# Optimization experiments

Measured on AMD Instinct MI355X. Metric: run time of the kernel, lower is better.

Reference implementation:

```python
import jax, jax.numpy as jnp
import numpy as np

N_FFT = 16
HOP = 4
PAD = N_FFT // 2  # center=True padding/trim, torch default


def _frame_idx(n_frames):
    # [n_frames, N_FFT] sample indices for framing / overlap-add
    return jnp.arange(n_frames)[:, None] * HOP + jnp.arange(N_FFT)[None, :]


def _istft(spec, window):
    # spec: complex [B, 9, T] onesided; matches torch.istft(center=True, onesided=True)
    B, _, T = spec.shape
    frames = jnp.fft.irfft(spec, n=N_FFT, axis=1)            # [B, 16, T]
    frames = jnp.transpose(frames, (0, 2, 1)) * window       # [B, T, 16] windowed
    idx = _frame_idx(T).reshape(-1)
    L = (T - 1) * HOP + N_FFT
    ola = jnp.zeros((B, L), frames.dtype).at[:, idx].add(frames.reshape(B, -1))
    wsq = jnp.broadcast_to(window**2, (T, N_FFT)).reshape(-1)
    env = jnp.zeros((L,), window.dtype).at[idx].add(wsq)      # window-square envelope
    Lout = (T - 1) * HOP                                      # torch output length, center=True
    return ola[:, PAD:PAD + Lout] / env[PAD:PAD + Lout]


def _stft(x, window):
    # matches torch.stft(center=True, pad_mode='reflect', onesided=True)
    B, L = x.shape
    xp = jnp.pad(x, ((0, 0), (PAD, PAD)), mode='reflect')
    T = 1 + L // HOP
    frames = xp[:, _frame_idx(T)] * window                    # [B, T, 16]
    return jnp.transpose(jnp.fft.rfft(frames, axis=-1), (0, 2, 1))  # [B, 9, T]


def _hann(n):
    k = jnp.arange(n, dtype=jnp.float32)
    return 0.5 * (1.0 - jnp.cos(2.0 * jnp.pi * k / n))  # periodic hann, torch default


def setup_inputs() -> dict:
    key = jax.random.key(0)
    magnitude = jax.random.uniform(key, (32, 9, 65536), dtype=jnp.float32)
    window = _hann(N_FFT)
    return {"magnitude": magnitude, "window": window}


def reference(magnitude, window):
    # 1) zero-phase istft
    spec0 = magnitude.astype(jnp.complex64)  # mag * exp(i*0)
    wav_i = _istft(spec0, window)
    # 2) stft -> extract phase
    S = _stft(wav_i, window)
    phase = jnp.arctan2(S.imag, S.real)      # torch.angle
    T = min(magnitude.shape[-1], phase.shape[-1])
    mag = magnitude[..., :T]
    ph = phase[..., :T]
    # 3) recombine and final istft
    spec = jax.lax.complex(mag * jnp.cos(ph), mag * jnp.sin(ph))
    return _istft(spec, window)
```

## Files before the change

kernel.cpp:

```cpp
#include <hip/hip_runtime.h>


#define KB    9
#define TFR   65536
#define LW    262140

#define C1f 0.9238795325112867f
#define C2f 0.7071067811865476f
#define C3f 0.3826834323650898f

#define W1 0.03806023374435663f
#define W2 0.14644660940672627f
#define W3 0.30865828381745514f
#define W4 0.5f
#define W5 0.6913417161825449f
#define W6 0.8535533905932737f
#define W7 0.9619397662556434f

#define TMIN   256
#define TMAX   65280
#define FPW    116
#define NWAVES 561
#define BXI    141
#define GX     (BXI + 2)
#define NBLK   (GX * 32)

#define TILE  1024
#define NW    1048
#define NCA   265
#define NFB   259
#define MSTR  265
#define FSTR  17
#define FSTEP (FSTR - 4)

typedef float v2f __attribute__((ext_vector_type(2)));
typedef float v4f __attribute__((ext_vector_type(4)));

static __device__ __forceinline__ v2f mk(float a, float b){ v2f r; r.x=a; r.y=b; return r; }
static __device__ __forceinline__ v2f sp(float c){ v2f r; r.x=c; r.y=c; return r; }
static __device__ __forceinline__ v2f vfma(v2f a, v2f b, v2f c){ return __builtin_elementwise_fma(a,b,c); }
static __device__ __forceinline__ v2f vfma(float a, v2f b, v2f c){ return __builtin_elementwise_fma(sp(a),b,c); }

static __device__ __forceinline__ float SHP(float x){
  int xi = __builtin_bit_cast(int, x);
  int r = __builtin_amdgcn_update_dpp(xi, xi, 0x130, 0xF, 0xF, false);
  return __builtin_bit_cast(float, r);
}
static __device__ __forceinline__ float SHM(float x){
  int xi = __builtin_bit_cast(int, x);
  int r = __builtin_amdgcn_update_dpp(xi, xi, 0x138, 0xF, 0xF, false);
  return __builtin_bit_cast(float, r);
}

static __device__ __forceinline__ void phase1(float m, float Sr, float Si,
                                              float& pr, float& pi){
  float r2 = fmaf(Sr,Sr, Si*Si);
  if (r2 > 0.f) {
    float rin = __builtin_amdgcn_rsqf(r2);
    float mr = m * rin;
    pr = mr * Sr; pi = mr * Si;
  } else { pr = m; pi = 0.f; }
}
static __device__ __forceinline__ void phasev(v2f m, v2f Sr, v2f Si, v2f& pr, v2f& pi){
  float prx, pix, pry, piy;
  phase1(m.x, Sr.x, Si.x, prx, pix);
  phase1(m.y, Sr.y, Si.y, pry, piy);
  pr = mk(prx, pry); pi = mk(pix, piy);
}

__device__ __constant__ float W2C[16] = {
  0.f, W1*W1, W2*W2, W3*W3, 0.25f, W5*W5, W6*W6, W7*W7,
  1.f, W7*W7, W6*W6, W5*W5, 0.25f, W3*W3, W2*W2, W1*W1 };

__global__ __launch_bounds__(256, 5) void istft_all(
    const float* __restrict__ mag, float* __restrict__ out)
{
  __shared__ float s_mag[KB * MSTR];
  __shared__ float s_fab[NCA * FSTR];
  __shared__ float s_wav[NW];

  const int tid = threadIdx.x;

  const unsigned lin = (unsigned)blockIdx.y * GX + blockIdx.x;
  const unsigned swz = (lin & 7u) * (NBLK / 8u) + (lin >> 3);
  const unsigned b   = swz / (unsigned)GX;
  const int      pos = (int)(swz - b * GX);

  const float* magb = mag + (size_t)b * (size_t)(KB * TFR);
  float* outb = out + (size_t)b * LW;

  if (pos >= 2) {
    const int lane = tid & 63;
    const int wv   = (pos - 2) * 4 + (tid >> 6);
    if (wv >= NWAVES) return;
    const int T0 = TMIN + wv * FPW;
    const int ta = T0 - 6 + 2 * lane;

    v2f R0 = *(const v2f*)(magb + 0*TFR + ta);
    v2f R1 = *(const v2f*)(magb + 1*TFR + ta);
    v2f R2 = *(const v2f*)(magb + 2*TFR + ta);
    v2f R3 = *(const v2f*)(magb + 3*TFR + ta);
    v2f R4 = *(const v2f*)(magb + 4*TFR + ta);
    v2f R5 = *(const v2f*)(magb + 5*TFR + ta);
    v2f R6 = *(const v2f*)(magb + 6*TFR + ta);
    v2f R7 = *(const v2f*)(magb + 7*TFR + ta);
    v2f R8 = *(const v2f*)(magb + 8*TFR + ta);

    v2f f1,f2,f3,f4,f5,f6,f7,f8;
    {
      v2f p1=R1+R7, m1=R1-R7, p2=R2+R6, m2=R2-R6, p3=R3+R5, m3=R3-R5;
      v2f tp=R0+R8, tm=R0-R8, d13=p1-p3;
      v2f E1 = vfma(2.f, vfma(C1f,m1, vfma(C2f,m2, sp(C3f)*m3)), tm);
      v2f E2 = vfma(2.f, vfma(C2f,d13, -R4), tp);
      v2f E3 = vfma(2.f, vfma(C3f,m1, vfma(-C2f,m2, sp(-C1f)*m3)), tm);
      v2f E4 = vfma(2.f, R4-p2, tp);
      v2f E5 = vfma(2.f, vfma(-C3f,m1, vfma(-C2f,m2, sp(C1f)*m3)), tm);
      v2f E6 = vfma(-2.f, vfma(C2f,d13, R4), tp);
      v2f E7 = vfma(2.f, vfma(-C1f,m1, vfma(C2f,m2, sp(-C3f)*m3)), tm);
      v2f E8 = vfma(2.f, ((p2+R4)-(p1+p3)), tp);
      f1=sp(W1)*E1; f2=sp(W2)*E2; f3=sp(W3)*E3; f4=sp(W4)*E4;
      f5=sp(W5)*E5; f6=sp(W6)*E6; f7=sp(W7)*E7; f8=E8;
    }

    v2f wc0, wc1, wc2, wc3;
    {
      float s4 = SHP(f4.x), s5 = SHP(f5.x), s6 = SHP(f6.x), s7 = SHP(f7.x);
      float a1x = SHP(f1.x), a1y = SHP(f1.y);
      float a2x = SHP(f2.x), a2y = SHP(f2.y);
      float a3x = SHP(f3.x), a3y = SHP(f3.y);
      float m1y = SHM(f1.y), m2y = SHM(f2.y), m3y = SHM(f3.y), m4y = SHM(f4.y);
      v2f f4p1 = mk(f4.y, s4), f5p1 = mk(f5.y, s5), f6p1 = mk(f6.y, s6), f7p1 = mk(f7.y, s7);
      v2f f1p2 = mk(a1x, a1y), f2p2 = mk(a2x, a2y), f3p2 = mk(a3x, a3y);
      v2f f1m1 = mk(m1y, f1.x), f2m1 = mk(m2y, f2.x), f3m1 = mk(m3y, f3.x), f4m1 = mk(m4y, f4.x);
      const v2f inv24 = sp(1.f/24.f);
      wc0 = (f4p1 + f8 + f4m1) * inv24;
      wc1 = (f1p2 + f5p1 + f7 + f3m1) * inv24;
      wc2 = (f2p2 + f6p1 + f6 + f2m1) * inv24;
      wc3 = (f3p2 + f7p1 + f5 + f1m1) * inv24;
    }

    v2f x1,x2,x3,x4,x5,x6,x7,x8w,x9,x10,x11,x12,x13,x14,x15;
    {
      float aw0y = SHM(wc0.y);
      float aw1x = SHM(wc1.x), aw1y = SHM(wc1.y);
      float aw2x = SHM(wc2.x), aw2y = SHM(wc2.y);
      float aw3x = SHM(wc3.x), aw3y = SHM(wc3.y);
      float pw0x = SHP(wc0.x), pw1x = SHP(wc1.x), pw2x = SHP(wc2.x), pw3x = SHP(wc3.x);
      x1  = mk(aw1x, aw1y); x2  = mk(aw2x, aw2y); x3  = mk(aw3x, aw3y);
      x4  = mk(aw0y, wc0.x); x5 = mk(aw1y, wc1.x); x6 = mk(aw2y, wc2.x); x7 = mk(aw3y, wc3.x);
      x8w = wc0; x9 = wc1; x10 = wc2; x11 = wc3;
      x12 = mk(wc0.y, pw0x); x13 = mk(wc1.y, pw1x); x14 = mk(wc2.y, pw2x); x15 = mk(wc3.y, pw3x);
    }
    x1=sp(W1)*x1; x2=sp(W2)*x2; x3=sp(W3)*x3; x4=sp(W4)*x4; x5=sp(W5)*x5;
    x6=sp(W6)*x6; x7=sp(W7)*x7; x9=sp(W7)*x9; x10=sp(W6)*x10; x11=sp(W5)*x11;
    x12=sp(W4)*x12; x13=sp(W3)*x13; x14=sp(W2)*x14; x15=sp(W1)*x15;

    v2f fc1,fc2,fc3,fc4,fc5,fc6,fc7,fc8,fc9,fc10,fc11,fc12,fc13,fc14,fc15;
    {
      v2f u1=x1+x15, vv1=x1-x15, u2=x2+x14, vv2=x2-x14, u3=x3+x13, vv3=x3-x13,
          u4=x4+x12, vv4=x4-x12, u5=x5+x11, vv5=x5-x11, u6=x6+x10, vv6=x6-x10,
          u7=x7+x9,  vv7=x7-x9;
      v2f P1=u1+u7, M1=u1-u7, P2=u2+u6, M2=u2-u6, P3=u3+u5, M3=u3-u5;
      v2f D13 = P1-P3;
      v2f Sr0 = x8w + ((P1+P2)+(P3+u4));
      v2f Sr1 = vfma(C1f,M1, vfma(C2f,M2, sp(C3f)*M3)) - x8w;
      v2f Sr2 = vfma(C2f,D13, x8w - u4);
      v2f Sr3 = vfma(C3f,M1, vfma(-C2f,M2, sp(-C1f)*M3)) - x8w;
      v2f Sr4 = (u4 - P2) + x8w;
      v2f Sr5 = vfma(-C3f,M1, vfma(-C2f,M2, sp(C1f)*M3)) - x8w;
      v2f Sr6 = vfma(-C2f,D13, x8w - u4);
      v2f Sr7 = vfma(-C1f,M1, vfma(C2f,M2, sp(-C3f)*M3)) - x8w;
      v2f Sr8 = x8w + ((P2+u4)-(P1+P3));
      v2f Q1=vv1+vv7, N1=vv1-vv7, Q2=vv2+vv6, N2=vv2-vv6, Q3=vv3+vv5, N3=vv3-vv5;
      v2f NN = N1+N3;
      v2f Si1 = -(vfma(C3f,Q1, vfma(C2f,Q2, sp(C1f)*Q3)) + vv4);
      v2f Si2 = -vfma(C2f,NN, N2);
      v2f Si3 = -(vfma(C1f,Q1, vfma(C2f,Q2, sp(-C3f)*Q3)) - vv4);
      v2f Si4 = N3 - N1;
      v2f Si5 = -(vfma(C1f,Q1, vfma(-C2f,Q2, sp(-C3f)*Q3)) + vv4);
      v2f Si6 = vfma(-C2f,NN, N2);
      v2f Si7 = -(vfma(C3f,Q1, vfma(-C2f,Q2, sp(C1f)*Q3)) - vv4);

      v2f pr0,pr1,pr2,pr3,pr4,pr5,pr6,pr7,pr8;
      v2f pi1,pi2,pi3,pi4,pi5,pi6,pi7;
      pr0 = mk((Sr0.x >= 0.f) ? R0.x : -R0.x,
               (Sr0.y >= 0.f) ? R0.y : -R0.y);
      phasev(R1, Sr1, Si1, pr1, pi1);
      phasev(R2, Sr2, Si2, pr2, pi2);
      phasev(R3, Sr3, Si3, pr3, pi3);
      phasev(R4, Sr4, Si4, pr4, pi4);
      phasev(R5, Sr5, Si5, pr5, pi5);
      phasev(R6, Sr6, Si6, pr6, pi6);
      phasev(R7, Sr7, Si7, pr7, pi7);
      pr8 = mk((Sr8.x >= 0.f) ? R8.x : -R8.x,
               (Sr8.y >= 0.f) ? R8.y : -R8.y);

      v2f ap1=pr1+pr7, bm1=pr1-pr7, ap2=pr2+pr6, bm2=pr2-pr6, ap3=pr3+pr5, bm3=pr3-pr5;
      v2f tp=pr0+pr8, tm=pr0-pr8, ed=ap1-ap3;
      v2f E1 = vfma(2.f, vfma(C1f,bm1, vfma(C2f,bm2, sp(C3f)*bm3)), tm);
      v2f E2 = vfma(2.f, vfma(C2f,ed, -pr4), tp);
      v2f E3 = vfma(2.f, vfma(C3f,bm1, vfma(-C2f,bm2, sp(-C1f)*bm3)), tm);
      v2f E4 = vfma(2.f, pr4-ap2, tp);
      v2f E5 = vfma(2.f, vfma(-C3f,bm1, vfma(-C2f,bm2, sp(C1f)*bm3)), tm);
      v2f E6 = vfma(-2.f, vfma(C2f,ed, pr4), tp);
      v2f E7 = vfma(2.f, vfma(-C1f,bm1, vfma(C2f,bm2, sp(-C3f)*bm3)), tm);
      v2f E8 = vfma(2.f, ((ap2+pr4)-(ap1+ap3)), tp);
      v2f q1=pi1+pi7, n1=pi1-pi7, q2=pi2+pi6, n2=pi2-pi6, q3=pi3+pi5, n3=pi3-pi5;
      v2f nn = n1+n3;
      v2f O1 = sp(-2.f)*(vfma(C3f,q1, vfma(C2f,q2, sp(C1f)*q3)) + pi4);
      v2f O2 = sp(-2.f)*vfma(C2f,nn, n2);
      v2f O3 = sp(-2.f)*(vfma(C1f,q1, vfma(C2f,q2, sp(-C3f)*q3)) - pi4);
      v2f O4 = sp(-2.f)*(n1-n3);
      v2f O5 = sp(-2.f)*(vfma(C1f,q1, vfma(-C2f,q2, sp(-C3f)*q3)) + pi4);
      v2f O6 = sp(-2.f)*vfma(C2f,nn, -n2);
      v2f O7 = sp(-2.f)*(vfma(C3f,q1, vfma(-C2f,q2, sp(C1f)*q3)) - pi4);

      fc1 = sp(W1)*(E1+O1); fc2 = sp(W2)*(E2+O2); fc3 = sp(W3)*(E3+O3); fc4 = sp(W4)*(E4+O4);
      fc5 = sp(W5)*(E5+O5); fc6 = sp(W6)*(E6+O6); fc7 = sp(W7)*(E7+O7); fc8 = E8;
      fc9  = sp(W7)*(E7-O7); fc10 = sp(W6)*(E6-O6); fc11 = sp(W5)*(E5-O5); fc12 = sp(W4)*(E4-O4);
      fc13 = sp(W3)*(E3-O3); fc14 = sp(W2)*(E2-O2); fc15 = sp(W1)*(E1-O1);
    }

    {
      float c1x = SHP(fc1.x), c1y = SHP(fc1.y);
      float c2x = SHP(fc2.x), c2y = SHP(fc2.y);
      float c3x = SHP(fc3.x), c3y = SHP(fc3.y);
      float c4x = SHP(fc4.x), c5x = SHP(fc5.x), c6x = SHP(fc6.x), c7x = SHP(fc7.x);
      float d12 = SHM(fc12.y), d13s = SHM(fc13.y), d14 = SHM(fc14.y), d15 = SHM(fc15.y);
      v2f g1 = mk(c1x, c1y), g2 = mk(c2x, c2y), g3 = mk(c3x, c3y);
      v2f h4 = mk(fc4.y, c4x), h5 = mk(fc5.y, c5x), h6 = mk(fc6.y, c6x), h7 = mk(fc7.y, c7x);
      v2f q12 = mk(d12, fc12.x), q13 = mk(d13s, fc13.x), q14 = mk(d14, fc14.x), q15 = mk(d15, fc15.x);
      const v2f inv24 = sp(1.f/24.f);
      v2f o0 = (h4 + fc8  + q12) * inv24;
      v2f o1 = (g1 + h5 + fc9  + q13) * inv24;
      v2f o2 = (g2 + h6 + fc10 + q14) * inv24;
      v2f o3 = (g3 + h7 + fc11 + q15) * inv24;
      if (lane >= 3 && lane <= 60 && ta < TMAX) {
        v4f s0 = {o0.x, o1.x, o2.x, o3.x};
        v4f s1 = {o0.y, o1.y, o2.y, o3.y};
        __builtin_nontemporal_store(s0, (v4f*)(outb + 4*(size_t)ta));
        __builtin_nontemporal_store(s1, (v4f*)(outb + 4*(size_t)ta + 4));
      }
    }
    return;
  }

  const int l0  = (pos == 0) ? 0 : 261120;
  const int t4  = l0 >> 2;
  const int tAlo = t4 - 4;
  const int tBlo = t4 - 1;
  const int wbase = l0 - 12;

#pragma unroll
  for (int k = 0; k < KB; ++k) {
    const float* mrow = magb + (size_t)k * TFR + tAlo;
    for (int c = tid; c < NCA; c += 256) {
      int t = tAlo + c;
      s_mag[k * MSTR + c] = ((unsigned)t < (unsigned)TFR) ? mrow[c] : 0.f;
    }
  }
  __syncthreads();

  for (int f = tid; f < NCA; f += 256) {
    float R0 = s_mag[0*MSTR+f], R1 = s_mag[1*MSTR+f], R2 = s_mag[2*MSTR+f],
          R3 = s_mag[3*MSTR+f], R4 = s_mag[4*MSTR+f], R5 = s_mag[5*MSTR+f],
          R6 = s_mag[6*MSTR+f], R7 = s_mag[7*MSTR+f], R8 = s_mag[8*MSTR+f];
    float p1=R1+R7, m1=R1-R7, p2=R2+R6, m2=R2-R6, p3=R3+R5, m3=R3-R5;
    float tp=R0+R8, tm=R0-R8, d13=p1-p3;
    float E1 = fmaf(2.f, fmaf(C1f,m1, fmaf(C2f,m2, C3f*m3)), tm);
    float E2 = fmaf(2.f, fmaf(C2f,d13, -R4), tp);
    float E3 = fmaf(2.f, fmaf(C3f,m1, fmaf(-C2f,m2, -C1f*m3)), tm);
    float E4 = fmaf(2.f, R4-p2, tp);
    float E5 = fmaf(2.f, fmaf(-C3f,m1, fmaf(-C2f,m2, C1f*m3)), tm);
    float E6 = fmaf(-2.f, fmaf(C2f,d13, R4), tp);
    float E7 = fmaf(2.f, fmaf(-C1f,m1, fmaf(C2f,m2, -C3f*m3)), tm);
    float E8 = fmaf(2.f, ((p2+R4)-(p1+p3)), tp);
    float* rp = s_fab + f * FSTR;
    rp[0]=0.f;    rp[1]=W1*E1;  rp[2]=W2*E2;  rp[3]=W3*E3;
    rp[4]=W4*E4;  rp[5]=W5*E5;  rp[6]=W6*E6;  rp[7]=W7*E7;
    rp[8]=E8;     rp[9]=W7*E7;  rp[10]=W6*E6; rp[11]=W5*E5;
    rp[12]=W4*E4; rp[13]=W3*E3; rp[14]=W2*E2; rp[15]=W1*E1;
  }
  __syncthreads();

  for (int i = tid; i < NW; i += 256) {
    int m = wbase + i;
    float val = 0.f;
    if (m >= 0 && m < LW) {
      int q = m + 8;
      int tq = q >> 2, r = q & 3;
      int base = (tq - tAlo) * FSTR + r;
      float acc = 0.f, env = 0.f;
#pragma unroll
      for (int j = 0; j < 4; ++j) {
        int t = tq - j;
        if ((unsigned)t < (unsigned)TFR) { acc += s_fab[base - FSTEP*j]; env += W2C[r + 4*j]; }
      }
      val = acc * __builtin_amdgcn_rcpf(16.f * env);
    }
    s_wav[i] = val;
  }
  __syncthreads();

  for (int f = tid; f < NFB; f += 256) {
    float* rp = s_fab + f * FSTR;
    int t2 = tBlo + f;
    bool valid = ((unsigned)t2 < (unsigned)TFR);
    if (valid) {
      float xs[16];
      int g0 = 4*t2 - 8;
#pragma unroll
      for (int n = 0; n < 16; ++n) {
        int g = g0 + n;
        g = (g < 0) ? -g : g;
        g = (g < LW) ? g : (2*(LW-1) - g);
        xs[n] = s_wav[g - wbase];
      }
      float x1=xs[1]*W1, x2=xs[2]*W2, x3=xs[3]*W3, x4=xs[4]*W4, x5=xs[5]*W5,
            x6=xs[6]*W6, x7=xs[7]*W7, x8w=xs[8], x9=xs[9]*W7, x10=xs[10]*W6,
            x11=xs[11]*W5, x12=xs[12]*W4, x13=xs[13]*W3, x14=xs[14]*W2, x15=xs[15]*W1;
      float u1=x1+x15, v1=x1-x15, u2=x2+x14, v2=x2-x14, u3=x3+x13, v3=x3-x13,
            u4=x4+x12, v4=x4-x12, u5=x5+x11, v5=x5-x11, u6=x6+x10, v6=x6-x10,
            u7=x7+x9,  v7=x7-x9;
      float P1=u1+u7, M1=u1-u7, P2=u2+u6, M2=u2-u6, P3=u3+u5, M3=u3-u5;
      float D13 = P1-P3;
      float Sr0 = x8w + ((P1+P2)+(P3+u4));
      float Sr1 = fmaf(C1f,M1, fmaf(C2f,M2, C3f*M3)) - x8w;
      float Sr2 = fmaf(C2f,D13, x8w - u4);
      float Sr3 = fmaf(C3f,M1, fmaf(-C2f,M2, -C1f*M3)) - x8w;
      float Sr4 = (u4 - P2) + x8w;
      float Sr5 = fmaf(-C3f,M1, fmaf(-C2f,M2, C1f*M3)) - x8w;
      float Sr6 = fmaf(-C2f,D13, x8w - u4);
      float Sr7 = fmaf(-C1f,M1, fmaf(C2f,M2, -C3f*M3)) - x8w;
      float Sr8 = x8w + ((P2+u4)-(P1+P3));
      float Q1=v1+v7, N1=v1-v7, Q2=v2+v6, N2=v2-v6, Q3=v3+v5, N3=v3-v5;
      float NN = N1+N3;
      float Si1 = -(fmaf(C3f,Q1, fmaf(C2f,Q2, C1f*Q3)) + v4);
      float Si2 = -fmaf(C2f,NN, N2);
      float Si3 = -(fmaf(C1f,Q1, fmaf(C2f,Q2, -C3f*Q3)) - v4);
      float Si4 = N3 - N1;
      float Si5 = -(fmaf(C1f,Q1, fmaf(-C2f,Q2, -C3f*Q3)) + v4);
      float Si6 = fmaf(-C2f,NN, N2);
      float Si7 = -(fmaf(C3f,Q1, fmaf(-C2f,Q2, C1f*Q3)) - v4);

      const float* mcol = s_mag + (f + 3);
      float pr0,pr1,pr2,pr3,pr4,pr5,pr6,pr7,pr8;
      float pi1,pi2,pi3,pi4,pi5,pi6,pi7;
      { float mm = mcol[0];
        pr0 = (Sr0 >= 0.f) ? mm : -mm; }
      phase1(mcol[1*MSTR], Sr1, Si1, pr1, pi1);
      phase1(mcol[2*MSTR], Sr2, Si2, pr2, pi2);
      phase1(mcol[3*MSTR], Sr3, Si3, pr3, pi3);
      phase1(mcol[4*MSTR], Sr4, Si4, pr4, pi4);
      phase1(mcol[5*MSTR], Sr5, Si5, pr5, pi5);
      phase1(mcol[6*MSTR], Sr6, Si6, pr6, pi6);
      phase1(mcol[7*MSTR], Sr7, Si7, pr7, pi7);
      { float mm = mcol[8*MSTR];
        pr8 = (Sr8 >= 0.f) ? mm : -mm; }

      float ap1=pr1+pr7, bm1=pr1-pr7, ap2=pr2+pr6, bm2=pr2-pr6, ap3=pr3+pr5, bm3=pr3-pr5;
      float tp=pr0+pr8, tm=pr0-pr8, ed=ap1-ap3;
      float E1 = fmaf(2.f, fmaf(C1f,bm1, fmaf(C2f,bm2, C3f*bm3)), tm);
      float E2 = fmaf(2.f, fmaf(C2f,ed, -pr4), tp);
      float E3 = fmaf(2.f, fmaf(C3f,bm1, fmaf(-C2f,bm2, -C1f*bm3)), tm);
      float E4 = fmaf(2.f, pr4-ap2, tp);
      float E5 = fmaf(2.f, fmaf(-C3f,bm1, fmaf(-C2f,bm2, C1f*bm3)), tm);
      float E6 = fmaf(-2.f, fmaf(C2f,ed, pr4), tp);
      float E7 = fmaf(2.f, fmaf(-C1f,bm1, fmaf(C2f,bm2, -C3f*bm3)), tm);
      float E8 = fmaf(2.f, ((ap2+pr4)-(ap1+ap3)), tp);
      float q1=pi1+pi7, n1=pi1-pi7, q2=pi2+pi6, n2=pi2-pi6, q3=pi3+pi5, n3=pi3-pi5;
      float nn = n1+n3;
      float O1 = -2.f*(fmaf(C3f,q1, fmaf(C2f,q2, C1f*q3)) + pi4);
      float O2 = -2.f*fmaf(C2f,nn, n2);
      float O3 = -2.f*(fmaf(C1f,q1, fmaf(C2f,q2, -C3f*q3)) - pi4);
      float O4 = -2.f*(n1-n3);
      float O5 = -2.f*(fmaf(C1f,q1, fmaf(-C2f,q2, -C3f*q3)) + pi4);
      float O6 = -2.f*fmaf(C2f,nn, -n2);
      float O7 = -2.f*(fmaf(C3f,q1, fmaf(-C2f,q2, C1f*q3)) - pi4);

      rp[0]=0.f;          rp[1]=W1*(E1+O1);  rp[2]=W2*(E2+O2);  rp[3]=W3*(E3+O3);
      rp[4]=W4*(E4+O4);   rp[5]=W5*(E5+O5);  rp[6]=W6*(E6+O6);  rp[7]=W7*(E7+O7);
      rp[8]=E8;           rp[9]=W7*(E7-O7);  rp[10]=W6*(E6-O6); rp[11]=W5*(E5-O5);
      rp[12]=W4*(E4-O4);  rp[13]=W3*(E3-O3); rp[14]=W2*(E2-O2); rp[15]=W1*(E1-O1);
    } else {
#pragma unroll
      for (int n = 0; n < 16; ++n) rp[n] = 0.f;
    }
  }
  __syncthreads();

  for (int i = tid; i < TILE; i += 256) {
    int l = l0 + i;
    if (l < LW) {
      int q = l + 8;
      int tq = q >> 2, r = q & 3;
      int base = (tq - tBlo) * FSTR + r;
      float acc = 0.f, env = 0.f;
#pragma unroll
      for (int j = 0; j < 4; ++j) {
        int t = tq - j;
        if ((unsigned)t < (unsigned)TFR) { acc += s_fab[base - FSTEP*j]; env += W2C[r + 4*j]; }
      }
      __builtin_nontemporal_store(acc * __builtin_amdgcn_rcpf(16.f * env), &outb[l]);
    }
  }
}

extern "C" void kernel_launch(void* const* d_in, const int* in_sizes, int n_in,
                              void* d_out, int out_size, void* d_ws, size_t ws_size,
                              hipStream_t stream) {
  const float* mag = (const float*)d_in[0];
  float* out = (float*)d_out;
  dim3 grid(GX, 32);
  istft_all<<<grid, 256, 0, stream>>>(mag, out);
}
```

Baseline: 120.8 us.

## Process four frames per lane to cut halo redundancy and cross-lane shuffles

Each lane now loads four consecutive frames with 128-bit loads, where it used to load two, and processes them as low and high halves. Neighbour exchange between the halves happens in registers, so fewer cross-lane shuffles are needed per frame. Each wave now covers 240 frames instead of 116, so the overlapping halo frames are a smaller share of the work. The cost is higher register pressure, which is why launch bounds drop to 3 waves per SIMD, and fewer waves overall means less latency hiding.

```diff
diff --git a/kernel.cpp b/kernel.cpp
--- a/kernel.cpp
+++ b/kernel.cpp
@@ -19,9 +19,9 @@
 
 #define TMIN   256
 #define TMAX   65280
-#define FPW    116
-#define NWAVES 561
-#define BXI    141
+#define FPW    240
+#define NWAVES 271
+#define BXI    68
 #define GX     (BXI + 2)
 #define NBLK   (GX * 32)
 
@@ -68,11 +68,153 @@
   pr = mk(prx, pry); pi = mk(pix, piy);
 }
 
+
+static __device__ __forceinline__ void stage_a(
+    v2f R0, v2f R1, v2f R2, v2f R3, v2f R4, v2f R5, v2f R6, v2f R7, v2f R8,
+    v2f& f1, v2f& f2, v2f& f3, v2f& f4, v2f& f5, v2f& f6, v2f& f7, v2f& f8)
+{
+  v2f p1=R1+R7, m1=R1-R7, p2=R2+R6, m2=R2-R6, p3=R3+R5, m3=R3-R5;
+  v2f tp=R0+R8, tm=R0-R8, d13=p1-p3;
+  v2f E1 = vfma(2.f, vfma(C1f,m1, vfma(C2f,m2, sp(C3f)*m3)), tm);
+  v2f E2 = vfma(2.f, vfma(C2f,d13, -R4), tp);
+  v2f E3 = vfma(2.f, vfma(C3f,m1, vfma(-C2f,m2, sp(-C1f)*m3)), tm);
+  v2f E4 = vfma(2.f, R4-p2, tp);
+  v2f E5 = vfma(2.f, vfma(-C3f,m1, vfma(-C2f,m2, sp(C1f)*m3)), tm);
+  v2f E6 = vfma(-2.f, vfma(C2f,d13, R4), tp);
+  v2f E7 = vfma(2.f, vfma(-C1f,m1, vfma(C2f,m2, sp(-C3f)*m3)), tm);
+  v2f E8 = vfma(2.f, ((p2+R4)-(p1+p3)), tp);
+  f1=sp(W1)*E1; f2=sp(W2)*E2; f3=sp(W3)*E3; f4=sp(W4)*E4;
+  f5=sp(W5)*E5; f6=sp(W6)*E6; f7=sp(W7)*E7; f8=E8;
+}
+
+static __device__ __forceinline__ void stage_a2(
+    v2f f1, v2f f2, v2f f3, v2f f4, v2f f5, v2f f6, v2f f7, v2f f8,
+    float s4, float s5, float s6, float s7,
+    float a1x, float a1y, float a2x, float a2y, float a3x, float a3y,
+    float m1y, float m2y, float m3y, float m4y,
+    v2f& wc0, v2f& wc1, v2f& wc2, v2f& wc3)
+{
+  v2f f4p1 = mk(f4.y, s4), f5p1 = mk(f5.y, s5), f6p1 = mk(f6.y, s6), f7p1 = mk(f7.y, s7);
+  v2f f1p2 = mk(a1x, a1y), f2p2 = mk(a2x, a2y), f3p2 = mk(a3x, a3y);
+  v2f f1m1 = mk(m1y, f1.x), f2m1 = mk(m2y, f2.x), f3m1 = mk(m3y, f3.x), f4m1 = mk(m4y, f4.x);
+  const v2f inv24 = sp(1.f/24.f);
+  wc0 = (f4p1 + f8 + f4m1) * inv24;
+  wc1 = (f1p2 + f5p1 + f7 + f3m1) * inv24;
+  wc2 = (f2p2 + f6p1 + f6 + f2m1) * inv24;
+  wc3 = (f3p2 + f7p1 + f5 + f1m1) * inv24;
+}
+
+static __device__ __forceinline__ void stage_bg(
+    v2f wc0, v2f wc1, v2f wc2, v2f wc3,
+    float aw0y, float aw1x, float aw1y, float aw2x, float aw2y, float aw3x, float aw3y,
+    float pw0x, float pw1x, float pw2x, float pw3x,
+    v2f& x1, v2f& x2, v2f& x3, v2f& x4, v2f& x5, v2f& x6, v2f& x7, v2f& x8w,
+    v2f& x9, v2f& x10, v2f& x11, v2f& x12, v2f& x13, v2f& x14, v2f& x15)
+{
+  x1  = mk(aw1x, aw1y); x2  = mk(aw2x, aw2y); x3  = mk(aw3x, aw3y);
+  x4  = mk(aw0y, wc0.x); x5 = mk(aw1y, wc1.x); x6 = mk(aw2y, wc2.x); x7 = mk(aw3y, wc3.x);
+  x8w = wc0; x9 = wc1; x10 = wc2; x11 = wc3;
+  x12 = mk(wc0.y, pw0x); x13 = mk(wc1.y, pw1x); x14 = mk(wc2.y, pw2x); x15 = mk(wc3.y, pw3x);
+}
+
+static __device__ __forceinline__ void middle(
+    v2f x1, v2f x2, v2f x3, v2f x4, v2f x5, v2f x6, v2f x7, v2f x8w,
+    v2f x9, v2f x10, v2f x11, v2f x12, v2f x13, v2f x14, v2f x15,
+    v2f R0, v2f R1, v2f R2, v2f R3, v2f R4, v2f R5, v2f R6, v2f R7, v2f R8,
+    v2f& fc1, v2f& fc2, v2f& fc3, v2f& fc4, v2f& fc5, v2f& fc6, v2f& fc7, v2f& fc8,
+    v2f& fc9, v2f& fc10, v2f& fc11, v2f& fc12, v2f& fc13, v2f& fc14, v2f& fc15)
+{
+  x1=sp(W1)*x1; x2=sp(W2)*x2; x3=sp(W3)*x3; x4=sp(W4)*x4; x5=sp(W5)*x5;
+  x6=sp(W6)*x6; x7=sp(W7)*x7; x9=sp(W7)*x9; x10=sp(W6)*x10; x11=sp(W5)*x11;
+  x12=sp(W4)*x12; x13=sp(W3)*x13; x14=sp(W2)*x14; x15=sp(W1)*x15;
+
+  v2f u1=x1+x15, vv1=x1-x15, u2=x2+x14, vv2=x2-x14, u3=x3+x13, vv3=x3-x13,
+      u4=x4+x12, vv4=x4-x12, u5=x5+x11, vv5=x5-x11, u6=x6+x10, vv6=x6-x10,
+      u7=x7+x9,  vv7=x7-x9;
+  v2f P1=u1+u7, M1=u1-u7, P2=u2+u6, M2=u2-u6, P3=u3+u5, M3=u3-u5;
+  v2f D13 = P1-P3;
+  v2f Sr0 = x8w + ((P1+P2)+(P3+u4));
+  v2f Sr1 = vfma(C1f,M1, vfma(C2f,M2, sp(C3f)*M3)) - x8w;
+  v2f Sr2 = vfma(C2f,D13, x8w - u4);
+  v2f Sr3 = vfma(C3f,M1, vfma(-C2f,M2, sp(-C1f)*M3)) - x8w;
+  v2f Sr4 = (u4 - P2) + x8w;
+  v2f Sr5 = vfma(-C3f,M1, vfma(-C2f,M2, sp(C1f)*M3)) - x8w;
+  v2f Sr6 = vfma(-C2f,D13, x8w - u4);
+  v2f Sr7 = vfma(-C1f,M1, vfma(C2f,M2, sp(-C3f)*M3)) - x8w;
+  v2f Sr8 = x8w + ((P2+u4)-(P1+P3));
+  v2f Q1=vv1+vv7, N1=vv1-vv7, Q2=vv2+vv6, N2=vv2-vv6, Q3=vv3+vv5, N3=vv3-vv5;
+  v2f NN = N1+N3;
+  v2f Si1 = -(vfma(C3f,Q1, vfma(C2f,Q2, sp(C1f)*Q3)) + vv4);
+  v2f Si2 = -vfma(C2f,NN, N2);
+  v2f Si3 = -(vfma(C1f,Q1, vfma(C2f,Q2, sp(-C3f)*Q3)) - vv4);
+  v2f Si4 = N3 - N1;
+  v2f Si5 = -(vfma(C1f,Q1, vfma(-C2f,Q2, sp(-C3f)*Q3)) + vv4);
+  v2f Si6 = vfma(-C2f,NN, N2);
+  v2f Si7 = -(vfma(C3f,Q1, vfma(-C2f,Q2, sp(C1f)*Q3)) - vv4);
+
+  v2f pr0,pr1,pr2,pr3,pr4,pr5,pr6,pr7,pr8;
+  v2f pi1,pi2,pi3,pi4,pi5,pi6,pi7;
+  pr0 = mk((Sr0.x >= 0.f) ? R0.x : -R0.x,
+           (Sr0.y >= 0.f) ? R0.y : -R0.y);
+  phasev(R1, Sr1, Si1, pr1, pi1);
+  phasev(R2, Sr2, Si2, pr2, pi2);
+  phasev(R3, Sr3, Si3, pr3, pi3);
+  phasev(R4, Sr4, Si4, pr4, pi4);
+  phasev(R5, Sr5, Si5, pr5, pi5);
+  phasev(R6, Sr6, Si6, pr6, pi6);
+  phasev(R7, Sr7, Si7, pr7, pi7);
+  pr8 = mk((Sr8.x >= 0.f) ? R8.x : -R8.x,
+           (Sr8.y >= 0.f) ? R8.y : -R8.y);
+
+  v2f ap1=pr1+pr7, bm1=pr1-pr7, ap2=pr2+pr6, bm2=pr2-pr6, ap3=pr3+pr5, bm3=pr3-pr5;
+  v2f tp=pr0+pr8, tm=pr0-pr8, ed=ap1-ap3;
+  v2f E1 = vfma(2.f, vfma(C1f,bm1, vfma(C2f,bm2, sp(C3f)*bm3)), tm);
+  v2f E2 = vfma(2.f, vfma(C2f,ed, -pr4), tp);
+  v2f E3 = vfma(2.f, vfma(C3f,bm1, vfma(-C2f,bm2, sp(-C1f)*bm3)), tm);
+  v2f E4 = vfma(2.f, pr4-ap2, tp);
+  v2f E5 = vfma(2.f, vfma(-C3f,bm1, vfma(-C2f,bm2, sp(C1f)*bm3)), tm);
+  v2f E6 = vfma(-2.f, vfma(C2f,ed, pr4), tp);
+  v2f E7 = vfma(2.f, vfma(-C1f,bm1, vfma(C2f,bm2, sp(-C3f)*bm3)), tm);
+  v2f E8 = vfma(2.f, ((ap2+pr4)-(ap1+ap3)), tp);
+  v2f q1=pi1+pi7, n1=pi1-pi7, q2=pi2+pi6, n2=pi2-pi6, q3=pi3+pi5, n3=pi3-pi5;
+  v2f nn = n1+n3;
+  v2f O1 = sp(-2.f)*(vfma(C3f,q1, vfma(C2f,q2, sp(C1f)*q3)) + pi4);
+  v2f O2 = sp(-2.f)*vfma(C2f,nn, n2);
+  v2f O3 = sp(-2.f)*(vfma(C1f,q1, vfma(C2f,q2, sp(-C3f)*q3)) - pi4);
+  v2f O4 = sp(-2.f)*(n1-n3);
+  v2f O5 = sp(-2.f)*(vfma(C1f,q1, vfma(-C2f,q2, sp(-C3f)*q3)) + pi4);
+  v2f O6 = sp(-2.f)*vfma(C2f,nn, -n2);
+  v2f O7 = sp(-2.f)*(vfma(C3f,q1, vfma(-C2f,q2, sp(C1f)*q3)) - pi4);
+
+  fc1 = sp(W1)*(E1+O1); fc2 = sp(W2)*(E2+O2); fc3 = sp(W3)*(E3+O3); fc4 = sp(W4)*(E4+O4);
+  fc5 = sp(W5)*(E5+O5); fc6 = sp(W6)*(E6+O6); fc7 = sp(W7)*(E7+O7); fc8 = E8;
+  fc9  = sp(W7)*(E7-O7); fc10 = sp(W6)*(E6-O6); fc11 = sp(W5)*(E5-O5); fc12 = sp(W4)*(E4-O4);
+  fc13 = sp(W3)*(E3-O3); fc14 = sp(W2)*(E2-O2); fc15 = sp(W1)*(E1-O1);
+}
+
+static __device__ __forceinline__ void stage_c(
+    v2f fc4, v2f fc5, v2f fc6, v2f fc7, v2f fc8, v2f fc9, v2f fc10, v2f fc11,
+    v2f fc12, v2f fc13, v2f fc14, v2f fc15,
+    float c1x, float c1y, float c2x, float c2y, float c3x, float c3y,
+    float c4x, float c5x, float c6x, float c7x,
+    float d12, float d13s, float d14, float d15,
+    v2f& o0, v2f& o1, v2f& o2, v2f& o3)
+{
+  v2f g1 = mk(c1x, c1y), g2 = mk(c2x, c2y), g3 = mk(c3x, c3y);
+  v2f h4 = mk(fc4.y, c4x), h5 = mk(fc5.y, c5x), h6 = mk(fc6.y, c6x), h7 = mk(fc7.y, c7x);
+  v2f q12 = mk(d12, fc12.x), q13 = mk(d13s, fc13.x), q14 = mk(d14, fc14.x), q15 = mk(d15, fc15.x);
+  const v2f inv24 = sp(1.f/24.f);
+  o0 = (h4 + fc8  + q12) * inv24;
+  o1 = (g1 + h5 + fc9  + q13) * inv24;
+  o2 = (g2 + h6 + fc10 + q14) * inv24;
+  o3 = (g3 + h7 + fc11 + q15) * inv24;
+}
+
 __device__ __constant__ float W2C[16] = {
   0.f, W1*W1, W2*W2, W3*W3, 0.25f, W5*W5, W6*W6, W7*W7,
   1.f, W7*W7, W6*W6, W5*W5, 0.25f, W3*W3, W2*W2, W1*W1 };
 
-__global__ __launch_bounds__(256, 5) void istft_all(
+__global__ __launch_bounds__(256, 3) void istft_all(
     const float* __restrict__ mag, float* __restrict__ out)
 {
   __shared__ float s_mag[KB * MSTR];
@@ -94,153 +236,87 @@
     const int wv   = (pos - 2) * 4 + (tid >> 6);
     if (wv >= NWAVES) return;
     const int T0 = TMIN + wv * FPW;
-    const int ta = T0 - 6 + 2 * lane;
-
-    v2f R0 = *(const v2f*)(magb + 0*TFR + ta);
-    v2f R1 = *(const v2f*)(magb + 1*TFR + ta);
-    v2f R2 = *(const v2f*)(magb + 2*TFR + ta);
-    v2f R3 = *(const v2f*)(magb + 3*TFR + ta);
-    v2f R4 = *(const v2f*)(magb + 4*TFR + ta);
-    v2f R5 = *(const v2f*)(magb + 5*TFR + ta);
-    v2f R6 = *(const v2f*)(magb + 6*TFR + ta);
-    v2f R7 = *(const v2f*)(magb + 7*TFR + ta);
-    v2f R8 = *(const v2f*)(magb + 8*TFR + ta);
-
-    v2f f1,f2,f3,f4,f5,f6,f7,f8;
-    {
-      v2f p1=R1+R7, m1=R1-R7, p2=R2+R6, m2=R2-R6, p3=R3+R5, m3=R3-R5;
-      v2f tp=R0+R8, tm=R0-R8, d13=p1-p3;
-      v2f E1 = vfma(2.f, vfma(C1f,m1, vfma(C2f,m2, sp(C3f)*m3)), tm);
-      v2f E2 = vfma(2.f, vfma(C2f,d13, -R4), tp);
-      v2f E3 = vfma(2.f, vfma(C3f,m1, vfma(-C2f,m2, sp(-C1f)*m3)), tm);
-      v2f E4 = vfma(2.f, R4-p2, tp);
-      v2f E5 = vfma(2.f, vfma(-C3f,m1, vfma(-C2f,m2, sp(C1f)*m3)), tm);
-      v2f E6 = vfma(-2.f, vfma(C2f,d13, R4), tp);
-      v2f E7 = vfma(2.f, vfma(-C1f,m1, vfma(C2f,m2, sp(-C3f)*m3)), tm);
-      v2f E8 = vfma(2.f, ((p2+R4)-(p1+p3)), tp);
-      f1=sp(W1)*E1; f2=sp(W2)*E2; f3=sp(W3)*E3; f4=sp(W4)*E4;
-      f5=sp(W5)*E5; f6=sp(W6)*E6; f7=sp(W7)*E7; f8=E8;
-    }
-
-    v2f wc0, wc1, wc2, wc3;
-    {
-      float s4 = SHP(f4.x), s5 = SHP(f5.x), s6 = SHP(f6.x), s7 = SHP(f7.x);
-      float a1x = SHP(f1.x), a1y = SHP(f1.y);
-      float a2x = SHP(f2.x), a2y = SHP(f2.y);
-      float a3x = SHP(f3.x), a3y = SHP(f3.y);
-      float m1y = SHM(f1.y), m2y = SHM(f2.y), m3y = SHM(f3.y), m4y = SHM(f4.y);
-      v2f f4p1 = mk(f4.y, s4), f5p1 = mk(f5.y, s5), f6p1 = mk(f6.y, s6), f7p1 = mk(f7.y, s7);
-      v2f f1p2 = mk(a1x, a1y), f2p2 = mk(a2x, a2y), f3p2 = mk(a3x, a3y);
-      v2f f1m1 = mk(m1y, f1.x), f2m1 = mk(m2y, f2.x), f3m1 = mk(m3y, f3.x), f4m1 = mk(m4y, f4.x);
-      const v2f inv24 = sp(1.f/24.f);
-      wc0 = (f4p1 + f8 + f4m1) * inv24;
-      wc1 = (f1p2 + f5p1 + f7 + f3m1) * inv24;
-      wc2 = (f2p2 + f6p1 + f6 + f2m1) * inv24;
-      wc3 = (f3p2 + f7p1 + f5 + f1m1) * inv24;
-    }
-
-    v2f x1,x2,x3,x4,x5,x6,x7,x8w,x9,x10,x11,x12,x13,x14,x15;
-    {
-      float aw0y = SHM(wc0.y);
-      float aw1x = SHM(wc1.x), aw1y = SHM(wc1.y);
-      float aw2x = SHM(wc2.x), aw2y = SHM(wc2.y);
-      float aw3x = SHM(wc3.x), aw3y = SHM(wc3.y);
-      float pw0x = SHP(wc0.x), pw1x = SHP(wc1.x), pw2x = SHP(wc2.x), pw3x = SHP(wc3.x);
-      x1  = mk(aw1x, aw1y); x2  = mk(aw2x, aw2y); x3  = mk(aw3x, aw3y);
-      x4  = mk(aw0y, wc0.x); x5 = mk(aw1y, wc1.x); x6 = mk(aw2y, wc2.x); x7 = mk(aw3y, wc3.x);
-      x8w = wc0; x9 = wc1; x10 = wc2; x11 = wc3;
-      x12 = mk(wc0.y, pw0x); x13 = mk(wc1.y, pw1x); x14 = mk(wc2.y, pw2x); x15 = mk(wc3.y, pw3x);
-    }
-    x1=sp(W1)*x1; x2=sp(W2)*x2; x3=sp(W3)*x3; x4=sp(W4)*x4; x5=sp(W5)*x5;
-    x6=sp(W6)*x6; x7=sp(W7)*x7; x9=sp(W7)*x9; x10=sp(W6)*x10; x11=sp(W5)*x11;
-    x12=sp(W4)*x12; x13=sp(W3)*x13; x14=sp(W2)*x14; x15=sp(W1)*x15;
-
-    v2f fc1,fc2,fc3,fc4,fc5,fc6,fc7,fc8,fc9,fc10,fc11,fc12,fc13,fc14,fc15;
-    {
-      v2f u1=x1+x15, vv1=x1-x15, u2=x2+x14, vv2=x2-x14, u3=x3+x13, vv3=x3-x13,
-          u4=x4+x12, vv4=x4-x12, u5=x5+x11, vv5=x5-x11, u6=x6+x10, vv6=x6-x10,
-          u7=x7+x9,  vv7=x7-x9;
-      v2f P1=u1+u7, M1=u1-u7, P2=u2+u6, M2=u2-u6, P3=u3+u5, M3=u3-u5;
-      v2f D13 = P1-P3;
-      v2f Sr0 = x8w + ((P1+P2)+(P3+u4));
-      v2f Sr1 = vfma(C1f,M1, vfma(C2f,M2, sp(C3f)*M3)) - x8w;
-      v2f Sr2 = vfma(C2f,D13, x8w - u4);
-      v2f Sr3 = vfma(C3f,M1, vfma(-C2f,M2, sp(-C1f)*M3)) - x8w;
-      v2f Sr4 = (u4 - P2) + x8w;
-      v2f Sr5 = vfma(-C3f,M1, vfma(-C2f,M2, sp(C1f)*M3)) - x8w;
-      v2f Sr6 = vfma(-C2f,D13, x8w - u4);
-      v2f Sr7 = vfma(-C1f,M1, vfma(C2f,M2, sp(-C3f)*M3)) - x8w;
-      v2f Sr8 = x8w + ((P2+u4)-(P1+P3));
-      v2f Q1=vv1+vv7, N1=vv1-vv7, Q2=vv2+vv6, N2=vv2-vv6, Q3=vv3+vv5, N3=vv3-vv5;
-      v2f NN = N1+N3;
-      v2f Si1 = -(vfma(C3f,Q1, vfma(C2f,Q2, sp(C1f)*Q3)) + vv4);
-      v2f Si2 = -vfma(C2f,NN, N2);
-      v2f Si3 = -(vfma(C1f,Q1, vfma(C2f,Q2, sp(-C3f)*Q3)) - vv4);
-      v2f Si4 = N3 - N1;
-      v2f Si5 = -(vfma(C1f,Q1, vfma(-C2f,Q2, sp(-C3f)*Q3)) + vv4);
-      v2f Si6 = vfma(-C2f,NN, N2);
-      v2f Si7 = -(vfma(C3f,Q1, vfma(-C2f,Q2, sp(C1f)*Q3)) - vv4);
-
-      v2f pr0,pr1,pr2,pr3,pr4,pr5,pr6,pr7,pr8;
-      v2f pi1,pi2,pi3,pi4,pi5,pi6,pi7;
-      pr0 = mk((Sr0.x >= 0.f) ? R0.x : -R0.x,
-               (Sr0.y >= 0.f) ? R0.y : -R0.y);
-      phasev(R1, Sr1, Si1, pr1, pi1);
-      phasev(R2, Sr2, Si2, pr2, pi2);
-      phasev(R3, Sr3, Si3, pr3, pi3);
-      phasev(R4, Sr4, Si4, pr4, pi4);
-      phasev(R5, Sr5, Si5, pr5, pi5);
-      phasev(R6, Sr6, Si6, pr6, pi6);
-      phasev(R7, Sr7, Si7, pr7, pi7);
-      pr8 = mk((Sr8.x >= 0.f) ? R8.x : -R8.x,
-               (Sr8.y >= 0.f) ? R8.y : -R8.y);
-
-      v2f ap1=pr1+pr7, bm1=pr1-pr7, ap2=pr2+pr6, bm2=pr2-pr6, ap3=pr3+pr5, bm3=pr3-pr5;
-      v2f tp=pr0+pr8, tm=pr0-pr8, ed=ap1-ap3;
-      v2f E1 = vfma(2.f, vfma(C1f,bm1, vfma(C2f,bm2, sp(C3f)*bm3)), tm);
-      v2f E2 = vfma(2.f, vfma(C2f,ed, -pr4), tp);
-      v2f E3 = vfma(2.f, vfma(C3f,bm1, vfma(-C2f,bm2, sp(-C1f)*bm3)), tm);
-      v2f E4 = vfma(2.f, pr4-ap2, tp);
-      v2f E5 = vfma(2.f, vfma(-C3f,bm1, vfma(-C2f,bm2, sp(C1f)*bm3)), tm);
-      v2f E6 = vfma(-2.f, vfma(C2f,ed, pr4), tp);
-      v2f E7 = vfma(2.f, vfma(-C1f,bm1, vfma(C2f,bm2, sp(-C3f)*bm3)), tm);
-      v2f E8 = vfma(2.f, ((ap2+pr4)-(ap1+ap3)), tp);
-      v2f q1=pi1+pi7, n1=pi1-pi7, q2=pi2+pi6, n2=pi2-pi6, q3=pi3+pi5, n3=pi3-pi5;
-      v2f nn = n1+n3;
-      v2f O1 = sp(-2.f)*(vfma(C3f,q1, vfma(C2f,q2, sp(C1f)*q3)) + pi4);
-      v2f O2 = sp(-2.f)*vfma(C2f,nn, n2);
-      v2f O3 = sp(-2.f)*(vfma(C1f,q1, vfma(C2f,q2, sp(-C3f)*q3)) - pi4);
-      v2f O4 = sp(-2.f)*(n1-n3);
-      v2f O5 = sp(-2.f)*(vfma(C1f,q1, vfma(-C2f,q2, sp(-C3f)*q3)) + pi4);
-      v2f O6 = sp(-2.f)*vfma(C2f,nn, -n2);
-      v2f O7 = sp(-2.f)*(vfma(C3f,q1, vfma(-C2f,q2, sp(C1f)*q3)) - pi4);
-
-      fc1 = sp(W1)*(E1+O1); fc2 = sp(W2)*(E2+O2); fc3 = sp(W3)*(E3+O3); fc4 = sp(W4)*(E4+O4);
-      fc5 = sp(W5)*(E5+O5); fc6 = sp(W6)*(E6+O6); fc7 = sp(W7)*(E7+O7); fc8 = E8;
-      fc9  = sp(W7)*(E7-O7); fc10 = sp(W6)*(E6-O6); fc11 = sp(W5)*(E5-O5); fc12 = sp(W4)*(E4-O4);
-      fc13 = sp(W3)*(E3-O3); fc14 = sp(W2)*(E2-O2); fc15 = sp(W1)*(E1-O1);
-    }
-
-    {
-      float c1x = SHP(fc1.x), c1y = SHP(fc1.y);
-      float c2x = SHP(fc2.x), c2y = SHP(fc2.y);
-      float c3x = SHP(fc3.x), c3y = SHP(fc3.y);
-      float c4x = SHP(fc4.x), c5x = SHP(fc5.x), c6x = SHP(fc6.x), c7x = SHP(fc7.x);
-      float d12 = SHM(fc12.y), d13s = SHM(fc13.y), d14 = SHM(fc14.y), d15 = SHM(fc15.y);
-      v2f g1 = mk(c1x, c1y), g2 = mk(c2x, c2y), g3 = mk(c3x, c3y);
-      v2f h4 = mk(fc4.y, c4x), h5 = mk(fc5.y, c5x), h6 = mk(fc6.y, c6x), h7 = mk(fc7.y, c7x);
-      v2f q12 = mk(d12, fc12.x), q13 = mk(d13s, fc13.x), q14 = mk(d14, fc14.x), q15 = mk(d15, fc15.x);
-      const v2f inv24 = sp(1.f/24.f);
-      v2f o0 = (h4 + fc8  + q12) * inv24;
-      v2f o1 = (g1 + h5 + fc9  + q13) * inv24;
-      v2f o2 = (g2 + h6 + fc10 + q14) * inv24;
-      v2f o3 = (g3 + h7 + fc11 + q15) * inv24;
-      if (lane >= 3 && lane <= 60 && ta < TMAX) {
-        v4f s0 = {o0.x, o1.x, o2.x, o3.x};
-        v4f s1 = {o0.y, o1.y, o2.y, o3.y};
-        __builtin_nontemporal_store(s0, (v4f*)(outb + 4*(size_t)ta));
-        __builtin_nontemporal_store(s1, (v4f*)(outb + 4*(size_t)ta + 4));
-      }
+    const int tb = T0 - 8 + 4 * lane;
+
+    const float* mp = magb + tb;
+    v4f Q0 = *(const v4f*)(mp + 0*TFR);
+    v4f Q1 = *(const v4f*)(mp + 1*TFR);
+    v4f Q2 = *(const v4f*)(mp + 2*TFR);
+    v4f Q3 = *(const v4f*)(mp + 3*TFR);
+    v4f Q4 = *(const v4f*)(mp + 4*TFR);
+    v4f Q5 = *(const v4f*)(mp + 5*TFR);
+    v4f Q6 = *(const v4f*)(mp + 6*TFR);
+    v4f Q7 = *(const v4f*)(mp + 7*TFR);
+    v4f Q8 = *(const v4f*)(mp + 8*TFR);
+    v2f RL0 = mk(Q0.x,Q0.y), RH0 = mk(Q0.z,Q0.w);
+    v2f RL1 = mk(Q1.x,Q1.y), RH1 = mk(Q1.z,Q1.w);
+    v2f RL2 = mk(Q2.x,Q2.y), RH2 = mk(Q2.z,Q2.w);
+    v2f RL3 = mk(Q3.x,Q3.y), RH3 = mk(Q3.z,Q3.w);
+    v2f RL4 = mk(Q4.x,Q4.y), RH4 = mk(Q4.z,Q4.w);
+    v2f RL5 = mk(Q5.x,Q5.y), RH5 = mk(Q5.z,Q5.w);
+    v2f RL6 = mk(Q6.x,Q6.y), RH6 = mk(Q6.z,Q6.w);
+    v2f RL7 = mk(Q7.x,Q7.y), RH7 = mk(Q7.z,Q7.w);
+    v2f RL8 = mk(Q8.x,Q8.y), RH8 = mk(Q8.z,Q8.w);
+
+    v2f fL1,fL2,fL3,fL4,fL5,fL6,fL7,fL8;
+    v2f fH1,fH2,fH3,fH4,fH5,fH6,fH7,fH8;
+    stage_a(RL0,RL1,RL2,RL3,RL4,RL5,RL6,RL7,RL8, fL1,fL2,fL3,fL4,fL5,fL6,fL7,fL8);
+    stage_a(RH0,RH1,RH2,RH3,RH4,RH5,RH6,RH7,RH8, fH1,fH2,fH3,fH4,fH5,fH6,fH7,fH8);
+
+    v2f wcL0,wcL1,wcL2,wcL3, wcH0,wcH1,wcH2,wcH3;
+    stage_a2(fL1,fL2,fL3,fL4,fL5,fL6,fL7,fL8,
+             fH4.x, fH5.x, fH6.x, fH7.x,
+             fH1.x, fH1.y, fH2.x, fH2.y, fH3.x, fH3.y,
+             SHM(fH1.y), SHM(fH2.y), SHM(fH3.y), SHM(fH4.y),
+             wcL0,wcL1,wcL2,wcL3);
+    stage_a2(fH1,fH2,fH3,fH4,fH5,fH6,fH7,fH8,
+             SHP(fL4.x), SHP(fL5.x), SHP(fL6.x), SHP(fL7.x),
+             SHP(fL1.x), SHP(fL1.y), SHP(fL2.x), SHP(fL2.y), SHP(fL3.x), SHP(fL3.y),
+             fL1.y, fL2.y, fL3.y, fL4.y,
+             wcH0,wcH1,wcH2,wcH3);
+
+    v2f xL1,xL2,xL3,xL4,xL5,xL6,xL7,xL8w,xL9,xL10,xL11,xL12,xL13,xL14,xL15;
+    v2f xH1,xH2,xH3,xH4,xH5,xH6,xH7,xH8w,xH9,xH10,xH11,xH12,xH13,xH14,xH15;
+    stage_bg(wcL0,wcL1,wcL2,wcL3,
+             SHM(wcH0.y), SHM(wcH1.x), SHM(wcH1.y), SHM(wcH2.x), SHM(wcH2.y), SHM(wcH3.x), SHM(wcH3.y),
+             wcH0.x, wcH1.x, wcH2.x, wcH3.x,
+             xL1,xL2,xL3,xL4,xL5,xL6,xL7,xL8w,xL9,xL10,xL11,xL12,xL13,xL14,xL15);
+    stage_bg(wcH0,wcH1,wcH2,wcH3,
+             wcL0.y, wcL1.x, wcL1.y, wcL2.x, wcL2.y, wcL3.x, wcL3.y,
+             SHP(wcL0.x), SHP(wcL1.x), SHP(wcL2.x), SHP(wcL3.x),
+             xH1,xH2,xH3,xH4,xH5,xH6,xH7,xH8w,xH9,xH10,xH11,xH12,xH13,xH14,xH15);
+
+    v2f fcL1,fcL2,fcL3,fcL4,fcL5,fcL6,fcL7,fcL8,fcL9,fcL10,fcL11,fcL12,fcL13,fcL14,fcL15;
+    v2f fcH1,fcH2,fcH3,fcH4,fcH5,fcH6,fcH7,fcH8,fcH9,fcH10,fcH11,fcH12,fcH13,fcH14,fcH15;
+    middle(xL1,xL2,xL3,xL4,xL5,xL6,xL7,xL8w,xL9,xL10,xL11,xL12,xL13,xL14,xL15,
+           RL0,RL1,RL2,RL3,RL4,RL5,RL6,RL7,RL8,
+           fcL1,fcL2,fcL3,fcL4,fcL5,fcL6,fcL7,fcL8,fcL9,fcL10,fcL11,fcL12,fcL13,fcL14,fcL15);
+    middle(xH1,xH2,xH3,xH4,xH5,xH6,xH7,xH8w,xH9,xH10,xH11,xH12,xH13,xH14,xH15,
+           RH0,RH1,RH2,RH3,RH4,RH5,RH6,RH7,RH8,
+           fcH1,fcH2,fcH3,fcH4,fcH5,fcH6,fcH7,fcH8,fcH9,fcH10,fcH11,fcH12,fcH13,fcH14,fcH15);
+
+    v2f oL0,oL1,oL2,oL3, oH0,oH1,oH2,oH3;
+    stage_c(fcL4,fcL5,fcL6,fcL7,fcL8,fcL9,fcL10,fcL11,fcL12,fcL13,fcL14,fcL15,
+            fcH1.x, fcH1.y, fcH2.x, fcH2.y, fcH3.x, fcH3.y,
+            fcH4.x, fcH5.x, fcH6.x, fcH7.x,
+            SHM(fcH12.y), SHM(fcH13.y), SHM(fcH14.y), SHM(fcH15.y),
+            oL0,oL1,oL2,oL3);
+    stage_c(fcH4,fcH5,fcH6,fcH7,fcH8,fcH9,fcH10,fcH11,fcH12,fcH13,fcH14,fcH15,
+            SHP(fcL1.x), SHP(fcL1.y), SHP(fcL2.x), SHP(fcL2.y), SHP(fcL3.x), SHP(fcL3.y),
+            SHP(fcL4.x), SHP(fcL5.x), SHP(fcL6.x), SHP(fcL7.x),
+            fcL12.y, fcL13.y, fcL14.y, fcL15.y,
+            oH0,oH1,oH2,oH3);
+
+    if (lane >= 2 && lane <= 61 && tb < TMAX) {
+      v4f s0 = {oL0.x,oL1.x,oL2.x,oL3.x};
+      v4f s1 = {oL0.y,oL1.y,oL2.y,oL3.y};
+      v4f s2 = {oH0.x,oH1.x,oH2.x,oH3.x};
+      v4f s3 = {oH0.y,oH1.y,oH2.y,oH3.y};
+      float* op = outb + 4*(size_t)tb;
+      __builtin_nontemporal_store(s0, (v4f*)op);
+      __builtin_nontemporal_store(s1, (v4f*)(op+4));
+      __builtin_nontemporal_store(s2, (v4f*)(op+8));
+      __builtin_nontemporal_store(s3, (v4f*)(op+12));
     }
     return;
   }
```

New measurement: 136.3 us. 12.8% more time.
